# Kernel tuning notes

Measured on AMD Instinct MI355X. Metric: run time of the kernel, lower is better.

The kernel has to match this reference:

```python
import jax, jax.numpy as jnp
import numpy as np

B, N, DIN, H, A = 4096, 32, 256, 128, 32  # batch, n_agents, din, hidden_dim, n_actions
NEG = 9e15


def _linear_params(key, fan_in, fan_out):
    kw, kb = jax.random.split(key)
    bound = 1.0 / np.sqrt(fan_in)
    w = jax.random.uniform(kw, (fan_in, fan_out), jnp.float32, -bound, bound)
    b = jax.random.uniform(kb, (fan_out,), jnp.float32, -bound, bound)
    return w, b


def setup_inputs() -> dict:
    key = jax.random.key(0)
    ks = jax.random.split(key, 12)
    x = jax.random.normal(ks[0], (B, N, DIN), jnp.float32)
    mask = jax.random.randint(ks[1], (B, N, N), 0, 2).astype(jnp.float32)
    enc_w, enc_b = _linear_params(ks[2], DIN, H)
    a1_vw, a1_vb = _linear_params(ks[3], H, H)
    a1_kw, a1_kb = _linear_params(ks[4], H, H)
    a1_qw, a1_qb = _linear_params(ks[5], H, H)
    a1_ow, a1_ob = _linear_params(ks[6], H, H)
    a2_vw, a2_vb = _linear_params(ks[7], H, H)
    a2_kw, a2_kb = _linear_params(ks[8], H, H)
    a2_qw, a2_qb = _linear_params(ks[9], H, H)
    a2_ow, a2_ob = _linear_params(ks[10], H, H)
    q_w, q_b = _linear_params(ks[11], H, A)
    return dict(x=x, mask=mask, enc_w=enc_w, enc_b=enc_b,
                a1_vw=a1_vw, a1_vb=a1_vb, a1_kw=a1_kw, a1_kb=a1_kb,
                a1_qw=a1_qw, a1_qb=a1_qb, a1_ow=a1_ow, a1_ob=a1_ob,
                a2_vw=a2_vw, a2_vb=a2_vb, a2_kw=a2_kw, a2_kb=a2_kb,
                a2_qw=a2_qw, a2_qb=a2_qb, a2_ow=a2_ow, a2_ob=a2_ob,
                q_w=q_w, q_b=q_b)


def _att_block(h, mask, vw, vb, kw, kb, qw, qb, ow, ob):
    # h: [B, N, H]; mask: [B, N, N]
    v = jax.nn.relu(jnp.einsum('bnd,dh->bnh', h, vw) + vb)
    q = jax.nn.relu(jnp.einsum('bnd,dh->bnh', h, qw) + qb)
    k = jax.nn.relu(jnp.einsum('bnd,dh->bnh', h, kw) + kb)
    scores = jnp.einsum('bih,bjh->bij', q, k)               # [B, N, N]
    logits = scores * mask - NEG * (1.0 - mask)
    att = jax.nn.softmax(logits, axis=2)
    out = jnp.einsum('bij,bjh->bih', att, v)
    return jax.nn.relu(jnp.einsum('bnh,ho->bno', out, ow) + ob)


def reference(x, mask, enc_w, enc_b,
              a1_vw, a1_vb, a1_kw, a1_kb, a1_qw, a1_qb, a1_ow, a1_ob,
              a2_vw, a2_vb, a2_kw, a2_kb, a2_qw, a2_qb, a2_ow, a2_ob,
              q_w, q_b):
    h1 = jax.nn.relu(jnp.einsum('bnd,dh->bnh', x, enc_w) + enc_b)
    h2 = _att_block(h1, mask, a1_vw, a1_vb, a1_kw, a1_kb, a1_qw, a1_qb, a1_ow, a1_ob)
    h3 = _att_block(h2, mask, a2_vw, a2_vb, a2_kw, a2_kb, a2_qw, a2_qb, a2_ow, a2_ob)
    q = jnp.einsum('bnh,ha->bna', h3, q_w) + q_b            # [B, N, A]
    return q
```

## Files before the change

kernel.cpp:

```cpp
#include <hip/hip_runtime.h>
#include <hip/hip_bf16.h>

typedef __attribute__((ext_vector_type(8))) short bf16x8;
typedef __attribute__((ext_vector_type(4))) short bf16x4;
typedef __attribute__((ext_vector_type(4))) float f32x4;

#define DEVI static __device__ __forceinline__

constexpr int NAG = 32, DIN = 256, HDIM = 128, ADIM = 32;

constexpr int WS_ENC = 0;
constexpr int WS_H   = 32768;
constexpr int WS_QW  = 32768 + 8 * 16384;

constexpr int L_P0 = 0, L_P1 = 8192, L_P2 = 16384, L_PV = 24576, L_TOT = 32768;

template<int ROWB>
DEVI int offR(int row, int bcol) {
  return row * ROWB + (((bcol >> 4) ^ (row & 15)) << 4) + (bcol & 15);
}
DEVI int offVA(int row, int bcol) {
  return row * 64 + (((bcol >> 4) ^ ((row >> 1) & 3)) << 4) + (bcol & 15);
}

DEVI short f2bf(float f) {
  union { float f; unsigned u; } a; a.f = f;
  return (short)((a.u + 0x7fffu + ((a.u >> 16) & 1u)) >> 16);
}

DEVI void sbar() {
  asm volatile("s_waitcnt lgkmcnt(0)\n\ts_barrier" ::: "memory");
}

__global__ void prep_weights(const float* __restrict__ enc_w,
                             const float* __restrict__ m0, const float* __restrict__ m1,
                             const float* __restrict__ m2, const float* __restrict__ m3,
                             const float* __restrict__ m4, const float* __restrict__ m5,
                             const float* __restrict__ m6, const float* __restrict__ m7,
                             const float* __restrict__ qw,
                             short* __restrict__ ws)
{
  const int blk = blockIdx.x, tid = threadIdx.x;
  const float* src; int base, NM, nsh, f4;
  if (blk < 32) { src = enc_w; base = WS_ENC; NM = 8; nsh = 7; f4 = blk * 256 + tid; }
  else if (blk < 160) {
    const int m = (blk - 32) >> 4;
    if      (m == 0) src = m0; else if (m == 1) src = m1;
    else if (m == 2) src = m2; else if (m == 3) src = m3;
    else if (m == 4) src = m4; else if (m == 5) src = m5;
    else if (m == 6) src = m6; else             src = m7;
    base = WS_H + (m << 14); NM = 8; nsh = 7; f4 = ((blk - 32) & 15) * 256 + tid;
  } else { src = qw; base = WS_QW; NM = 2; nsh = 5; f4 = (blk - 160) * 256 + tid; }
  const int s = f4 * 4;
  const int row = s >> nsh, col0 = s & ((1 << nsh) - 1);
  const float4 v = *(const float4*)(src + s);
  const int j = row & 7, ks = row >> 5, lhi = ((row >> 3) & 3) * 16;
  const float vv[4] = {v.x, v.y, v.z, v.w};
#pragma unroll
  for (int c = 0; c < 4; ++c) {
    const int col = col0 + c;
    const int mt = col >> 4, lane = lhi + (col & 15);
    ws[base + (((ks * NM + mt) * 64 + lane) << 3) + j] = f2bf(vv[c]);
  }
}

template<int KSTEPS, bool RELU, int SRB>
DEVI void linearSw4(const char* __restrict__ src,
                    const short* __restrict__ wfrag, const float* __restrict__ bias,
                    char* __restrict__ dst,
                    int mg, int lr, int lq, int lane)
{
  f32x4 acc[2][2];
#pragma unroll
  for (int a = 0; a < 2; ++a)
#pragma unroll
    for (int b = 0; b < 2; ++b) acc[a][b] = (f32x4){0.f, 0.f, 0.f, 0.f};

  const bf16x8* wp = (const bf16x8*)wfrag;
  __builtin_amdgcn_s_setprio(1);
#pragma unroll
  for (int ks = 0; ks < KSTEPS; ++ks) {
    bf16x8 hb[2];
#pragma unroll
    for (int b = 0; b < 2; ++b)
      hb[b] = *(const bf16x8*)(src + offR<SRB>(b * 16 + lr, ks * 64 + lq * 16));
#pragma unroll
    for (int a = 0; a < 2; ++a) {
      const bf16x8 wa = wp[(ks * 8 + mg * 2 + a) * 64 + lane];
#pragma unroll
      for (int b = 0; b < 2; ++b)
        acc[a][b] = __builtin_amdgcn_mfma_f32_16x16x32_bf16(wa, hb[b], acc[a][b], 0, 0, 0);
    }
  }
  __builtin_amdgcn_s_setprio(0);
#pragma unroll
  for (int a = 0; a < 2; ++a) {
    const float4 bv = *(const float4*)(bias + (mg * 2 + a) * 16 + lq * 4);
    const float bb[4] = {bv.x, bv.y, bv.z, bv.w};
#pragma unroll
    for (int b = 0; b < 2; ++b) {
      bf16x4 s;
#pragma unroll
      for (int r = 0; r < 4; ++r) {
        float v = acc[a][b][r] + bb[r];
        if (RELU) v = fmaxf(v, 0.f);
        s[r] = f2bf(v);
      }
      *(bf16x4*)(dst + offR<256>(b * 16 + lr, (mg * 2 + a) * 32 + lq * 8)) = s;
    }
  }
}

DEVI void qkv_pass4(const char* __restrict__ h,
                    const short* __restrict__ wq, const short* __restrict__ wk,
                    const short* __restrict__ wv,
                    const float* __restrict__ bq, const float* __restrict__ bk,
                    const float* __restrict__ bv,
                    char* __restrict__ Q, char* __restrict__ K, char* __restrict__ V,
                    int mg, int lr, int lq, int lane)
{
  f32x4 qa[2][2], ka[2][2], va[2][2];
#pragma unroll
  for (int a = 0; a < 2; ++a)
#pragma unroll
    for (int b = 0; b < 2; ++b) {
      qa[a][b] = (f32x4){0.f, 0.f, 0.f, 0.f};
      ka[a][b] = (f32x4){0.f, 0.f, 0.f, 0.f};
      va[a][b] = (f32x4){0.f, 0.f, 0.f, 0.f};
    }
  const bf16x8* wpq = (const bf16x8*)wq;
  const bf16x8* wpk = (const bf16x8*)wk;
  const bf16x8* wpv = (const bf16x8*)wv;
  __builtin_amdgcn_s_setprio(1);
#pragma unroll
  for (int ks = 0; ks < 4; ++ks) {
    bf16x8 hf[2];
#pragma unroll
    for (int b = 0; b < 2; ++b)
      hf[b] = *(const bf16x8*)(h + offR<256>(b * 16 + lr, ks * 64 + lq * 16));
#pragma unroll
    for (int a = 0; a < 2; ++a) {
      const bf16x8 wqf = wpq[(ks * 8 + mg * 2 + a) * 64 + lane];
      const bf16x8 wkf = wpk[(ks * 8 + mg * 2 + a) * 64 + lane];
      const bf16x8 wvf = wpv[(ks * 8 + mg * 2 + a) * 64 + lane];
#pragma unroll
      for (int b = 0; b < 2; ++b) {
        qa[a][b] = __builtin_amdgcn_mfma_f32_16x16x32_bf16(wqf, hf[b], qa[a][b], 0, 0, 0);
        ka[a][b] = __builtin_amdgcn_mfma_f32_16x16x32_bf16(wkf, hf[b], ka[a][b], 0, 0, 0);
        va[b][a] = __builtin_amdgcn_mfma_f32_16x16x32_bf16(hf[b], wvf, va[b][a], 0, 0, 0);
      }
    }
  }
  __builtin_amdgcn_s_setprio(0);
#pragma unroll
  for (int a = 0; a < 2; ++a) {
    const float4 bq4 = *(const float4*)(bq + (mg * 2 + a) * 16 + lq * 4);
    const float4 bk4 = *(const float4*)(bk + (mg * 2 + a) * 16 + lq * 4);
    const float qb4[4] = {bq4.x, bq4.y, bq4.z, bq4.w};
    const float kb4[4] = {bk4.x, bk4.y, bk4.z, bk4.w};
#pragma unroll
    for (int b = 0; b < 2; ++b) {
      bf16x4 sq, sk;
#pragma unroll
      for (int r = 0; r < 4; ++r) {
        sq[r] = f2bf(fmaxf(qa[a][b][r] + qb4[r], 0.f));
        sk[r] = f2bf(fmaxf(ka[a][b][r] + kb4[r], 0.f));
      }
      const int off = offR<256>(b * 16 + lr, (mg * 2 + a) * 32 + lq * 8);
      *(bf16x4*)(Q + off) = sq;
      *(bf16x4*)(K + off) = sk;
    }
  }
#pragma unroll
  for (int a = 0; a < 2; ++a) {
    const float bvv = bv[(mg * 2 + a) * 16 + lr];
#pragma unroll
    for (int b = 0; b < 2; ++b) {
      bf16x4 sv;
#pragma unroll
      for (int r = 0; r < 4; ++r)
        sv[r] = f2bf(fmaxf(va[b][a][r] + bvv, 0.f));
      *(bf16x4*)(V + offVA((mg * 2 + a) * 16 + lr, b * 32 + lq * 8)) = sv;
    }
  }
}

DEVI void scores_pass4(const char* __restrict__ Q, const char* __restrict__ K,
                       char* __restrict__ AT,
                       unsigned mb, int qt, int lr, int lq)
{
  f32x4 sc[2];
  sc[0] = (f32x4){0.f, 0.f, 0.f, 0.f};
  sc[1] = (f32x4){0.f, 0.f, 0.f, 0.f};
  __builtin_amdgcn_s_setprio(1);
#pragma unroll
  for (int ks = 0; ks < 4; ++ks) {
    const bf16x8 qf = *(const bf16x8*)(Q + offR<256>(qt * 16 + lr, ks * 64 + lq * 16));
#pragma unroll
    for (int kt = 0; kt < 2; ++kt) {
      const bf16x8 kf = *(const bf16x8*)(K + offR<256>(kt * 16 + lr, ks * 64 + lq * 16));
      sc[kt] = __builtin_amdgcn_mfma_f32_16x16x32_bf16(kf, qf, sc[kt], 0, 0, 0);
    }
  }
  __builtin_amdgcn_s_setprio(0);
  float l[2][4];
  float M = -3.0e38f;
#pragma unroll
  for (int kt = 0; kt < 2; ++kt)
#pragma unroll
    for (int r = 0; r < 4; ++r) {
      const float v = ((mb >> (kt * 4 + r)) & 1u) ? sc[kt][r] : -9.0e15f;
      l[kt][r] = v;
      M = fmaxf(M, v);
    }
  M = fmaxf(M, __shfl_xor(M, 16));
  M = fmaxf(M, __shfl_xor(M, 32));
  float e[2][4], T = 0.f;
#pragma unroll
  for (int kt = 0; kt < 2; ++kt)
#pragma unroll
    for (int r = 0; r < 4; ++r) { e[kt][r] = __expf(l[kt][r] - M); T += e[kt][r]; }
  T += __shfl_xor(T, 16);
  T += __shfl_xor(T, 32);
  const float rT = __frcp_rn(T);
#pragma unroll
  for (int kt = 0; kt < 2; ++kt) {
    bf16x4 s;
#pragma unroll
    for (int r = 0; r < 4; ++r) s[r] = f2bf(e[kt][r] * rT);
    *(bf16x4*)(AT + offVA(qt * 16 + lr, kt * 32 + lq * 8)) = s;
  }
}

DEVI void pv_pass4(const char* __restrict__ V, const char* __restrict__ AT,
                   char* __restrict__ AO, int wave, int lr, int lq)
{
  bf16x8 atf[2];
#pragma unroll
  for (int qt = 0; qt < 2; ++qt)
    atf[qt] = *(const bf16x8*)(AT + offVA(qt * 16 + lr, lq * 16));
  __builtin_amdgcn_s_setprio(1);
#pragma unroll
  for (int fi = 0; fi < 2; ++fi) {
    const int f2 = wave * 2 + fi;
    const bf16x8 vf = *(const bf16x8*)(V + offVA(f2 * 16 + lr, lq * 16));
#pragma unroll
    for (int qt = 0; qt < 2; ++qt) {
      const f32x4 p = __builtin_amdgcn_mfma_f32_16x16x32_bf16(
          vf, atf[qt], (f32x4){0.f, 0.f, 0.f, 0.f}, 0, 0, 0);
      bf16x4 s;
#pragma unroll
      for (int r = 0; r < 4; ++r) s[r] = f2bf(p[r]);
      *(bf16x4*)(AO + offR<256>(qt * 16 + lr, f2 * 32 + lq * 8)) = s;
    }
  }
  __builtin_amdgcn_s_setprio(0);
}

DEVI void att_block4(const char* Rh, char* RQ, char* RK, char* RV,
                     char* RAT, char* RAO, char* Rout,
                     const short* wv, const short* wk, const short* wq, const short* wo,
                     const float* bv, const float* bk, const float* bq, const float* bo,
                     unsigned mb, int wave, int lr, int lq, int lane)
{
  qkv_pass4(Rh, wq, wk, wv, bq, bk, bv, RQ, RK, RV, wave, lr, lq, lane);
  sbar();
  if (wave < 2) scores_pass4(RQ, RK, RAT, mb, wave, lr, lq);
  sbar();
  pv_pass4(RV, RAT, RAO, wave, lr, lq);
  sbar();
  linearSw4<4, true, 256>(RAO, wo, bo, Rout, wave, lr, lq, lane);
  sbar();
}

__global__ __launch_bounds__(256, 4)
void dgn_main(const float* __restrict__ x, const float* __restrict__ mask,
              const float* __restrict__ enc_b,
              const float* __restrict__ b1v, const float* __restrict__ b1k,
              const float* __restrict__ b1q, const float* __restrict__ b1o,
              const float* __restrict__ b2v, const float* __restrict__ b2k,
              const float* __restrict__ b2q, const float* __restrict__ b2o,
              const float* __restrict__ qb,
              const short* __restrict__ wf,
              float* __restrict__ out)
{
  __shared__ __align__(16) char smem[L_TOT];
  char* P0 = smem + L_P0;
  char* P1 = smem + L_P1;
  char* P2 = smem + L_P2;
  char* PV = smem + L_PV;
  char* XB = smem + L_P1;

  const int tid = threadIdx.x;
  const int wave = tid >> 6, lane = tid & 63;
  const int lr = lane & 15, lq = lane >> 4;
  const int b0 = blockIdx.x;

  unsigned mb = 0;
  if (wave < 2) {
    const float* mp = mask + (size_t)b0 * (NAG * NAG) + (wave * 16 + lr) * 32 + lq * 4;
    const float4 m40 = *(const float4*)(mp);
    const float4 m41 = *(const float4*)(mp + 16);
    const float mm[8] = {m40.x, m40.y, m40.z, m40.w, m41.x, m41.y, m41.z, m41.w};
#pragma unroll
    for (int i = 0; i < 8; ++i)
      if (mm[i] != 0.f) mb |= 1u << i;
  }

  {
    const float4* xsrc = (const float4*)(x + (size_t)b0 * NAG * DIN);
#pragma unroll
    for (int it = 0; it < 8; ++it) {
      const int q4 = tid + it * 256;
      const float4 v = xsrc[q4];
      bf16x4 s;
      s[0] = f2bf(v.x); s[1] = f2bf(v.y); s[2] = f2bf(v.z); s[3] = f2bf(v.w);
      *(bf16x4*)(XB + offR<512>(q4 >> 6, (q4 & 63) * 8)) = s;
    }
  }
  sbar();

  linearSw4<8, true, 512>(XB, wf + WS_ENC, enc_b, P0, wave, lr, lq, lane);
  sbar();

  att_block4(P0, P1, P2, PV, P0, P1, P2,
             wf + WS_H + 0 * 16384, wf + WS_H + 1 * 16384,
             wf + WS_H + 2 * 16384, wf + WS_H + 3 * 16384,
             b1v, b1k, b1q, b1o, mb, wave, lr, lq, lane);

  att_block4(P2, P0, P1, PV, P2, P0, P1,
             wf + WS_H + 4 * 16384, wf + WS_H + 5 * 16384,
             wf + WS_H + 6 * 16384, wf + WS_H + 7 * 16384,
             b2v, b2k, b2q, b2o, mb, wave, lr, lq, lane);

  {
    const int at = wave >> 1, agt = wave & 1;
    f32x4 ha = (f32x4){0.f, 0.f, 0.f, 0.f};
    const bf16x8* wp = (const bf16x8*)(wf + WS_QW);
#pragma unroll
    for (int ks = 0; ks < 4; ++ks) {
      const bf16x8 hf = *(const bf16x8*)(P1 + offR<256>(agt * 16 + lr, ks * 64 + lq * 16));
      ha = __builtin_amdgcn_mfma_f32_16x16x32_bf16(wp[(ks * 2 + at) * 64 + lane], hf, ha, 0, 0, 0);
    }
    const float4 bv4 = *(const float4*)(qb + at * 16 + lq * 4);
    float* op = out + ((size_t)b0 * NAG + agt * 16 + lr) * ADIM;
    float4 o;
    o.x = ha[0] + bv4.x; o.y = ha[1] + bv4.y;
    o.z = ha[2] + bv4.z; o.w = ha[3] + bv4.w;
    *(float4*)(op + at * 16 + lq * 4) = o;
  }
}

extern "C" void kernel_launch(void* const* d_in, const int* in_sizes, int n_in,
                              void* d_out, int out_size, void* d_ws, size_t ws_size,
                              hipStream_t stream)
{
  const float* x     = (const float*)d_in[0];
  const float* mask  = (const float*)d_in[1];
  const float* enc_w = (const float*)d_in[2];
  const float* enc_b = (const float*)d_in[3];
  const float* a1_vw = (const float*)d_in[4];
  const float* a1_vb = (const float*)d_in[5];
  const float* a1_kw = (const float*)d_in[6];
  const float* a1_kb = (const float*)d_in[7];
  const float* a1_qw = (const float*)d_in[8];
  const float* a1_qb = (const float*)d_in[9];
  const float* a1_ow = (const float*)d_in[10];
  const float* a1_ob = (const float*)d_in[11];
  const float* a2_vw = (const float*)d_in[12];
  const float* a2_vb = (const float*)d_in[13];
  const float* a2_kw = (const float*)d_in[14];
  const float* a2_kb = (const float*)d_in[15];
  const float* a2_qw = (const float*)d_in[16];
  const float* a2_qb = (const float*)d_in[17];
  const float* a2_ow = (const float*)d_in[18];
  const float* a2_ob = (const float*)d_in[19];
  const float* q_w   = (const float*)d_in[20];
  const float* q_b   = (const float*)d_in[21];
  short* ws = (short*)d_ws;

  prep_weights<<<164, 256, 0, stream>>>(
      enc_w, a1_vw, a1_kw, a1_qw, a1_ow, a2_vw, a2_kw, a2_qw, a2_ow, q_w, ws);

  dgn_main<<<4096, 256, 0, stream>>>(
      x, mask, enc_b,
      a1_vb, a1_kb, a1_qb, a1_ob,
      a2_vb, a2_kb, a2_qb, a2_ob,
      q_b, ws, (float*)d_out);
}
```

Measured before the change: 300.6 us.

## Split QKV projection into two phases, drop setprio, and raise occupancy

The fused Q/K/V projection loop becomes two sequential phases, Q+K first and then V, which cuts the number of live accumulators and so the register pressure. Launch bounds go from 4 to 5 blocks per CU to allow more concurrent workgroups. The custom s_waitcnt+s_barrier is replaced with __syncthreads, all s_setprio hints are removed, and the final Q-head projection now runs on two waves with two accumulators each instead of all four waves. The trade-off is that the h fragments are read from LDS twice and fewer waves do the final GEMM, while tighter register limits could cause spills.

```diff
diff --git a/kernel.cpp b/kernel.cpp
--- a/kernel.cpp
+++ b/kernel.cpp
@@ -26,10 +26,6 @@
 DEVI short f2bf(float f) {
   union { float f; unsigned u; } a; a.f = f;
   return (short)((a.u + 0x7fffu + ((a.u >> 16) & 1u)) >> 16);
-}
-
-DEVI void sbar() {
-  asm volatile("s_waitcnt lgkmcnt(0)\n\ts_barrier" ::: "memory");
 }
 
 __global__ void prep_weights(const float* __restrict__ enc_w,
@@ -77,7 +73,6 @@
     for (int b = 0; b < 2; ++b) acc[a][b] = (f32x4){0.f, 0.f, 0.f, 0.f};
 
   const bf16x8* wp = (const bf16x8*)wfrag;
-  __builtin_amdgcn_s_setprio(1);
 #pragma unroll
   for (int ks = 0; ks < KSTEPS; ++ks) {
     bf16x8 hb[2];
@@ -92,7 +87,6 @@
         acc[a][b] = __builtin_amdgcn_mfma_f32_16x16x32_bf16(wa, hb[b], acc[a][b], 0, 0, 0);
     }
   }
-  __builtin_amdgcn_s_setprio(0);
 #pragma unroll
   for (int a = 0; a < 2; ++a) {
     const float4 bv = *(const float4*)(bias + (mg * 2 + a) * 16 + lq * 4);
@@ -119,80 +113,97 @@
                     char* __restrict__ Q, char* __restrict__ K, char* __restrict__ V,
                     int mg, int lr, int lq, int lane)
 {
-  f32x4 qa[2][2], ka[2][2], va[2][2];
-#pragma unroll
-  for (int a = 0; a < 2; ++a)
-#pragma unroll
-    for (int b = 0; b < 2; ++b) {
-      qa[a][b] = (f32x4){0.f, 0.f, 0.f, 0.f};
-      ka[a][b] = (f32x4){0.f, 0.f, 0.f, 0.f};
-      va[a][b] = (f32x4){0.f, 0.f, 0.f, 0.f};
-    }
-  const bf16x8* wpq = (const bf16x8*)wq;
-  const bf16x8* wpk = (const bf16x8*)wk;
-  const bf16x8* wpv = (const bf16x8*)wv;
-  __builtin_amdgcn_s_setprio(1);
-#pragma unroll
-  for (int ks = 0; ks < 4; ++ks) {
-    bf16x8 hf[2];
-#pragma unroll
-    for (int b = 0; b < 2; ++b)
-      hf[b] = *(const bf16x8*)(h + offR<256>(b * 16 + lr, ks * 64 + lq * 16));
+  {
+    f32x4 qa[2][2], ka[2][2];
+#pragma unroll
+    for (int a = 0; a < 2; ++a)
+#pragma unroll
+      for (int b = 0; b < 2; ++b) {
+        qa[a][b] = (f32x4){0.f, 0.f, 0.f, 0.f};
+        ka[a][b] = (f32x4){0.f, 0.f, 0.f, 0.f};
+      }
+    const bf16x8* wpq = (const bf16x8*)wq;
+    const bf16x8* wpk = (const bf16x8*)wk;
+#pragma unroll
+    for (int ks = 0; ks < 4; ++ks) {
+      bf16x8 hf[2];
+#pragma unroll
+      for (int b = 0; b < 2; ++b)
+        hf[b] = *(const bf16x8*)(h + offR<256>(b * 16 + lr, ks * 64 + lq * 16));
+#pragma unroll
+      for (int a = 0; a < 2; ++a) {
+        const bf16x8 wqf = wpq[(ks * 8 + mg * 2 + a) * 64 + lane];
+        const bf16x8 wkf = wpk[(ks * 8 + mg * 2 + a) * 64 + lane];
+#pragma unroll
+        for (int b = 0; b < 2; ++b) {
+          qa[a][b] = __builtin_amdgcn_mfma_f32_16x16x32_bf16(wqf, hf[b], qa[a][b], 0, 0, 0);
+          ka[a][b] = __builtin_amdgcn_mfma_f32_16x16x32_bf16(wkf, hf[b], ka[a][b], 0, 0, 0);
+        }
+      }
+    }
 #pragma unroll
     for (int a = 0; a < 2; ++a) {
-      const bf16x8 wqf = wpq[(ks * 8 + mg * 2 + a) * 64 + lane];
-      const bf16x8 wkf = wpk[(ks * 8 + mg * 2 + a) * 64 + lane];
-      const bf16x8 wvf = wpv[(ks * 8 + mg * 2 + a) * 64 + lane];
+      const float4 bq4 = *(const float4*)(bq + (mg * 2 + a) * 16 + lq * 4);
+      const float4 bk4 = *(const float4*)(bk + (mg * 2 + a) * 16 + lq * 4);
+      const float qb4[4] = {bq4.x, bq4.y, bq4.z, bq4.w};
+      const float kb4[4] = {bk4.x, bk4.y, bk4.z, bk4.w};
 #pragma unroll
       for (int b = 0; b < 2; ++b) {
-        qa[a][b] = __builtin_amdgcn_mfma_f32_16x16x32_bf16(wqf, hf[b], qa[a][b], 0, 0, 0);
-        ka[a][b] = __builtin_amdgcn_mfma_f32_16x16x32_bf16(wkf, hf[b], ka[a][b], 0, 0, 0);
-        va[b][a] = __builtin_amdgcn_mfma_f32_16x16x32_bf16(hf[b], wvf, va[b][a], 0, 0, 0);
-      }
-    }
-  }
-  __builtin_amdgcn_s_setprio(0);
-#pragma unroll
-  for (int a = 0; a < 2; ++a) {
-    const float4 bq4 = *(const float4*)(bq + (mg * 2 + a) * 16 + lq * 4);
-    const float4 bk4 = *(const float4*)(bk + (mg * 2 + a) * 16 + lq * 4);
-    const float qb4[4] = {bq4.x, bq4.y, bq4.z, bq4.w};
-    const float kb4[4] = {bk4.x, bk4.y, bk4.z, bk4.w};
-#pragma unroll
-    for (int b = 0; b < 2; ++b) {
-      bf16x4 sq, sk;
-#pragma unroll
-      for (int r = 0; r < 4; ++r) {
-        sq[r] = f2bf(fmaxf(qa[a][b][r] + qb4[r], 0.f));
-        sk[r] = f2bf(fmaxf(ka[a][b][r] + kb4[r], 0.f));
-      }
-      const int off = offR<256>(b * 16 + lr, (mg * 2 + a) * 32 + lq * 8);
-      *(bf16x4*)(Q + off) = sq;
-      *(bf16x4*)(K + off) = sk;
-    }
-  }
-#pragma unroll
-  for (int a = 0; a < 2; ++a) {
-    const float bvv = bv[(mg * 2 + a) * 16 + lr];
-#pragma unroll
-    for (int b = 0; b < 2; ++b) {
-      bf16x4 sv;
-#pragma unroll
-      for (int r = 0; r < 4; ++r)
-        sv[r] = f2bf(fmaxf(va[b][a][r] + bvv, 0.f));
-      *(bf16x4*)(V + offVA((mg * 2 + a) * 16 + lr, b * 32 + lq * 8)) = sv;
+        bf16x4 sq, sk;
+#pragma unroll
+        for (int r = 0; r < 4; ++r) {
+          sq[r] = f2bf(fmaxf(qa[a][b][r] + qb4[r], 0.f));
+          sk[r] = f2bf(fmaxf(ka[a][b][r] + kb4[r], 0.f));
+        }
+        const int off = offR<256>(b * 16 + lr, (mg * 2 + a) * 32 + lq * 8);
+        *(bf16x4*)(Q + off) = sq;
+        *(bf16x4*)(K + off) = sk;
+      }
+    }
+  }
+  {
+    f32x4 va[2][2];
+#pragma unroll
+    for (int a = 0; a < 2; ++a)
+#pragma unroll
+      for (int b = 0; b < 2; ++b) va[b][a] = (f32x4){0.f, 0.f, 0.f, 0.f};
+    const bf16x8* wpv = (const bf16x8*)wv;
+#pragma unroll
+    for (int ks = 0; ks < 4; ++ks) {
+      bf16x8 hf[2];
+#pragma unroll
+      for (int b = 0; b < 2; ++b)
+        hf[b] = *(const bf16x8*)(h + offR<256>(b * 16 + lr, ks * 64 + lq * 16));
+#pragma unroll
+      for (int a = 0; a < 2; ++a) {
+        const bf16x8 wvf = wpv[(ks * 8 + mg * 2 + a) * 64 + lane];
+#pragma unroll
+        for (int b = 0; b < 2; ++b)
+          va[b][a] = __builtin_amdgcn_mfma_f32_16x16x32_bf16(hf[b], wvf, va[b][a], 0, 0, 0);
+      }
+    }
+#pragma unroll
+    for (int a = 0; a < 2; ++a) {
+      const float bvv = bv[(mg * 2 + a) * 16 + lr];
+#pragma unroll
+      for (int b = 0; b < 2; ++b) {
+        bf16x4 sv;
+#pragma unroll
+        for (int r = 0; r < 4; ++r)
+          sv[r] = f2bf(fmaxf(va[b][a][r] + bvv, 0.f));
+        *(bf16x4*)(V + offVA((mg * 2 + a) * 16 + lr, b * 32 + lq * 8)) = sv;
+      }
     }
   }
 }
 
 DEVI void scores_pass4(const char* __restrict__ Q, const char* __restrict__ K,
-                       char* __restrict__ AT,
-                       unsigned mb, int qt, int lr, int lq)
+                       char* __restrict__ AT, unsigned mb,
+                       int qt, int lr, int lq)
 {
   f32x4 sc[2];
   sc[0] = (f32x4){0.f, 0.f, 0.f, 0.f};
   sc[1] = (f32x4){0.f, 0.f, 0.f, 0.f};
-  __builtin_amdgcn_s_setprio(1);
 #pragma unroll
   for (int ks = 0; ks < 4; ++ks) {
     const bf16x8 qf = *(const bf16x8*)(Q + offR<256>(qt * 16 + lr, ks * 64 + lq * 16));
@@ -202,7 +213,6 @@
       sc[kt] = __builtin_amdgcn_mfma_f32_16x16x32_bf16(kf, qf, sc[kt], 0, 0, 0);
     }
   }
-  __builtin_amdgcn_s_setprio(0);
   float l[2][4];
   float M = -3.0e38f;
 #pragma unroll
@@ -239,7 +249,6 @@
 #pragma unroll
   for (int qt = 0; qt < 2; ++qt)
     atf[qt] = *(const bf16x8*)(AT + offVA(qt * 16 + lr, lq * 16));
-  __builtin_amdgcn_s_setprio(1);
 #pragma unroll
   for (int fi = 0; fi < 2; ++fi) {
     const int f2 = wave * 2 + fi;
@@ -254,7 +263,6 @@
       *(bf16x4*)(AO + offR<256>(qt * 16 + lr, f2 * 32 + lq * 8)) = s;
     }
   }
-  __builtin_amdgcn_s_setprio(0);
 }
 
 DEVI void att_block4(const char* Rh, char* RQ, char* RK, char* RV,
@@ -264,16 +272,16 @@
                      unsigned mb, int wave, int lr, int lq, int lane)
 {
   qkv_pass4(Rh, wq, wk, wv, bq, bk, bv, RQ, RK, RV, wave, lr, lq, lane);
-  sbar();
+  __syncthreads();
   if (wave < 2) scores_pass4(RQ, RK, RAT, mb, wave, lr, lq);
-  sbar();
+  __syncthreads();
   pv_pass4(RV, RAT, RAO, wave, lr, lq);
-  sbar();
+  __syncthreads();
   linearSw4<4, true, 256>(RAO, wo, bo, Rout, wave, lr, lq, lane);
-  sbar();
-}
-
-__global__ __launch_bounds__(256, 4)
+  __syncthreads();
+}
+
+__global__ __launch_bounds__(256, 5)
 void dgn_main(const float* __restrict__ x, const float* __restrict__ mask,
               const float* __restrict__ enc_b,
               const float* __restrict__ b1v, const float* __restrict__ b1k,
@@ -318,10 +326,10 @@
       *(bf16x4*)(XB + offR<512>(q4 >> 6, (q4 & 63) * 8)) = s;
     }
   }
-  sbar();
+  __syncthreads();
 
   linearSw4<8, true, 512>(XB, wf + WS_ENC, enc_b, P0, wave, lr, lq, lane);
-  sbar();
+  __syncthreads();
 
   att_block4(P0, P1, P2, PV, P0, P1, P2,
              wf + WS_H + 0 * 16384, wf + WS_H + 1 * 16384,
@@ -333,21 +341,27 @@
              wf + WS_H + 6 * 16384, wf + WS_H + 7 * 16384,
              b2v, b2k, b2q, b2o, mb, wave, lr, lq, lane);
 
-  {
-    const int at = wave >> 1, agt = wave & 1;
-    f32x4 ha = (f32x4){0.f, 0.f, 0.f, 0.f};
+  if (wave < 2) {
+    f32x4 ha[2];
+    ha[0] = (f32x4){0.f, 0.f, 0.f, 0.f};
+    ha[1] = (f32x4){0.f, 0.f, 0.f, 0.f};
     const bf16x8* wp = (const bf16x8*)(wf + WS_QW);
 #pragma unroll
     for (int ks = 0; ks < 4; ++ks) {
-      const bf16x8 hf = *(const bf16x8*)(P1 + offR<256>(agt * 16 + lr, ks * 64 + lq * 16));
-      ha = __builtin_amdgcn_mfma_f32_16x16x32_bf16(wp[(ks * 2 + at) * 64 + lane], hf, ha, 0, 0, 0);
-    }
-    const float4 bv4 = *(const float4*)(qb + at * 16 + lq * 4);
-    float* op = out + ((size_t)b0 * NAG + agt * 16 + lr) * ADIM;
-    float4 o;
-    o.x = ha[0] + bv4.x; o.y = ha[1] + bv4.y;
-    o.z = ha[2] + bv4.z; o.w = ha[3] + bv4.w;
-    *(float4*)(op + at * 16 + lq * 4) = o;
+      const bf16x8 hf = *(const bf16x8*)(P1 + offR<256>(wave * 16 + lr, ks * 64 + lq * 16));
+#pragma unroll
+      for (int a = 0; a < 2; ++a)
+        ha[a] = __builtin_amdgcn_mfma_f32_16x16x32_bf16(wp[(ks * 2 + a) * 64 + lane], hf, ha[a], 0, 0, 0);
+    }
+    float* op = out + ((size_t)b0 * NAG + wave * 16 + lr) * ADIM;
+#pragma unroll
+    for (int a = 0; a < 2; ++a) {
+      const float4 bv4 = *(const float4*)(qb + a * 16 + lq * 4);
+      float4 o;
+      o.x = ha[a][0] + bv4.x; o.y = ha[a][1] + bv4.y;
+      o.z = ha[a][2] + bv4.z; o.w = ha[a][3] + bv4.w;
+      *(float4*)(op + a * 16 + lq * 4) = o;
+    }
   }
 }
 
```

Result: slower. 393.2 us (+30.8%).
